# Kernel tuning notes

Hardware: AMD Instinct MI355X
Metric: run time of the kernel (lower is better)

Reference implementation:

```python
import jax, jax.numpy as jnp
import numpy as np

DOWNSAMPLE = 1  # downsample_factor


def _grid(out_h, out_w):
    # rows: x in [-1,1] along width, y in [-1,1] along height, ones
    x_t = jnp.linspace(-1.0, 1.0, out_w, dtype=jnp.float32)
    y_t = jnp.linspace(-1.0, 1.0, out_h, dtype=jnp.float32)
    xg = jnp.tile(x_t[None, :], (out_h, 1)).reshape(-1)
    yg = jnp.tile(y_t[:, None], (1, out_w)).reshape(-1)
    return jnp.stack([xg, yg, jnp.ones_like(xg)], axis=0)  # [3, P]


def spatial_transform(X, theta):
    B, C, H, W = X.shape
    out_h, out_w = H // DOWNSAMPLE, W // DOWNSAMPLE
    grid = _grid(out_h, out_w)                               # [3, P]
    Tg = jnp.einsum('bij,jp->bip', theta.reshape(B, 2, 3), grid)  # [B,2,P]
    x_s, y_s = Tg[:, 0], Tg[:, 1]                            # [B, P]

    # map from [-1,1] to pixel coords (same convention as original)
    x = (x_s + 1.0) * (W / 2.0)
    y = (y_s + 1.0) * (H / 2.0)
    x0 = jnp.floor(x).astype(jnp.int32)
    x1 = x0 + 1
    y0 = jnp.floor(y).astype(jnp.int32)
    y1 = y0 + 1
    x0c = jnp.clip(x0, 0, W - 1)
    x1c = jnp.clip(x1, 0, W - 1)
    y0c = jnp.clip(y0, 0, H - 1)
    y1c = jnp.clip(y1, 0, H - 1)

    im = jnp.transpose(X, (0, 2, 3, 1)).reshape(B, H * W, C)  # [B, HW, C]

    def gather(yi, xi):
        idx = yi * W + xi                                      # [B, P]
        return jnp.take_along_axis(im, idx[:, :, None], axis=1)  # [B, P, C]

    Ia = gather(y0c, x0c)
    Ib = gather(y1c, x0c)
    Ic = gather(y0c, x1c)
    Id = gather(y1c, x1c)

    x0f = x0c.astype(jnp.float32)
    x1f = x1c.astype(jnp.float32)
    y0f = y0c.astype(jnp.float32)
    y1f = y1c.astype(jnp.float32)
    wa = ((x1f - x) * (y1f - y))[:, :, None]
    wb = ((x1f - x) * (y - y0f))[:, :, None]
    wc = ((x - x0f) * (y1f - y))[:, :, None]
    wd = ((x - x0f) * (y - y0f))[:, :, None]

    out = wa * Ia + wb * Ib + wc * Ic + wd * Id               # [B, P, C]
    out = out.reshape(B, out_h, out_w, C)
    return jnp.transpose(out, (0, 3, 1, 2))                   # NCHW


def setup_inputs() -> dict:
    key = jax.random.key(0)
    kx, kt = jax.random.split(key)
    X = jax.random.normal(kx, (32, 3, 512, 512), dtype=jnp.float32)
    # theta near identity + noise for sensible transforms
    ident = jnp.array([1.0, 0.0, 0.0, 0.0, 1.0, 0.0], dtype=jnp.float32)
    theta = ident[None, :] + 0.1 * jax.random.normal(kt, (32, 6), dtype=jnp.float32)
    return {"X": X, "theta": theta}


def reference(X, theta):
    return spatial_transform(X, theta)
```

## Files before the change

### kernel.cpp

```cpp
#include <hip/hip_runtime.h>


#define ST_H 512
#define ST_W 512
#define ST_C 3
#define ST_HW (ST_H * ST_W)

typedef float f2 __attribute__((ext_vector_type(2)));
struct __attribute__((packed, aligned(4))) f2_a4 { f2 v; };

__global__ __launch_bounds__(256) void st_bilinear_kernel(
    const float* __restrict__ X,
    const float* __restrict__ theta,
    float* __restrict__ out,
    int chunk)
{
    int bid = blockIdx.x;
    bid = (bid & 7) * chunk + (bid >> 3);

    const int b   = bid >> 9;
    const int idx = bid & 511;
    const int tx  = idx & 7;
    const int ty  = idx >> 3;

    const int tid = (int)threadIdx.x;
    const int w  = (tx << 6) + (tid & 63);
    const int r  = tid >> 6;
    const int h1 = (ty << 3) + r;
    const int h2 = h1 + 4;

    const float* t = theta + b * 6;
    const float t00 = t[0], t01 = t[1], t02 = t[2];
    const float t10 = t[3], t11 = t[4], t12 = t[5];

    const float STEP = (float)(2.0 / 511.0);
    const float xg  = fmaf((float)w, STEP, -1.0f);
    const float xb0 = fmaf(t00, xg, t02);
    const float yb0 = fmaf(t10, xg, t12);

    const float* __restrict__ Xb = X + (size_t)b * (ST_C * ST_HW);
    float* __restrict__ ob = out + (size_t)b * (ST_C * ST_HW) + w;

#pragma unroll
    for (int k = 0; k < 2; ++k) {
        const int h = k ? h2 : h1;
        const float yg = fmaf((float)h, STEP, -1.0f);
        const float x = (fmaf(t01, yg, xb0) + 1.0f) * 256.0f;
        const float y = (fmaf(t11, yg, yb0) + 1.0f) * 256.0f;

        const int x0 = (int)floorf(x);
        const int y0 = (int)floorf(y);

        const int x0c = min(max(x0, 0), ST_W - 1);
        const int x1c = min(max(x0 + 1, 0), ST_W - 1);
        const int y0c = min(max(y0, 0), ST_H - 1);
        const int y1c = min(max(y0 + 1, 0), ST_H - 1);

        const float x0f = (float)x0c, x1f = (float)x1c;
        const float y0f = (float)y0c, y1f = (float)y1c;
        const float wa = (x1f - x) * (y1f - y);
        const float wb = (x1f - x) * (y - y0f);
        const float wc = (x - x0f) * (y1f - y);
        const float wd = (x - x0f) * (y - y0f);

        const int xa = min(max(x0, 0), ST_W - 2);
        const bool hi = (x0 >= ST_W - 1);
        const bool lo = (x0 < 0);

        const int ia = y0c * ST_W + xa;
        const int ib = y1c * ST_W + xa;

        float* __restrict__ o = ob + h * ST_W;
#pragma unroll
        for (int c = 0; c < ST_C; ++c) {
            const float* __restrict__ Xc = Xb + c * ST_HW;
            const f2 p = ((const f2_a4*)(Xc + ia))->v;
            const f2 q = ((const f2_a4*)(Xc + ib))->v;
            const float Ia = hi ? p.y : p.x;
            const float Ic = lo ? p.x : p.y;
            const float Ib = hi ? q.y : q.x;
            const float Id = lo ? q.x : q.y;
            const float v = wa * Ia + wb * Ib + wc * Ic + wd * Id;
            __builtin_nontemporal_store(v, o + c * ST_HW);
        }
    }
}

extern "C" void kernel_launch(void* const* d_in, const int* in_sizes, int n_in,
                              void* d_out, int out_size, void* d_ws, size_t ws_size,
                              hipStream_t stream) {
    const float* X     = (const float*)d_in[0];
    const float* theta = (const float*)d_in[1];
    float* out         = (float*)d_out;

    const int B = in_sizes[1] / 6;
    const int block = 256;
    const int grid = B * 512;
    const int chunk = grid / 8;

    st_bilinear_kernel<<<grid, block, 0, stream>>>(X, theta, out, chunk);
}
```

Before: 39.40 us.

## Stage output tile in LDS and write with 128-bit nontemporal stores

Each block now covers a 64x16 output tile instead of 64x8, with four rows per thread, and halves the grid. Results are written into shared memory first and then stored to global memory as float4 nontemporal stores, replacing the scalar per-channel stores. The goal is fewer, wider store transactions and fewer blocks, at the cost of 12 KB of LDS per block, a __syncthreads barrier, and less store overlap with the gather loads.

After: 40.97 us. 4.0% more time.

```diff
diff --git a/kernel.cpp b/kernel.cpp
--- a/kernel.cpp
+++ b/kernel.cpp
@@ -7,6 +7,7 @@
 #define ST_HW (ST_H * ST_W)
 
 typedef float f2 __attribute__((ext_vector_type(2)));
+typedef float f4 __attribute__((ext_vector_type(4)));
 struct __attribute__((packed, aligned(4))) f2_a4 { f2 v; };
 
 __global__ __launch_bounds__(256) void st_bilinear_kernel(
@@ -15,19 +16,21 @@
     float* __restrict__ out,
     int chunk)
 {
+    __shared__ float sb[ST_C * 16 * 64];
+
     int bid = blockIdx.x;
     bid = (bid & 7) * chunk + (bid >> 3);
 
-    const int b   = bid >> 9;
-    const int idx = bid & 511;
+    const int b   = bid >> 8;
+    const int idx = bid & 255;
     const int tx  = idx & 7;
     const int ty  = idx >> 3;
+    const int hb  = ty << 4;
 
-    const int tid = (int)threadIdx.x;
-    const int w  = (tx << 6) + (tid & 63);
-    const int r  = tid >> 6;
-    const int h1 = (ty << 3) + r;
-    const int h2 = h1 + 4;
+    const int tid  = (int)threadIdx.x;
+    const int lane = tid & 63;
+    const int r    = tid >> 6;
+    const int w    = (tx << 6) + lane;
 
     const float* t = theta + b * 6;
     const float t00 = t[0], t01 = t[1], t02 = t[2];
@@ -39,11 +42,11 @@
     const float yb0 = fmaf(t10, xg, t12);
 
     const float* __restrict__ Xb = X + (size_t)b * (ST_C * ST_HW);
-    float* __restrict__ ob = out + (size_t)b * (ST_C * ST_HW) + w;
 
 #pragma unroll
-    for (int k = 0; k < 2; ++k) {
-        const int h = k ? h2 : h1;
+    for (int k = 0; k < 4; ++k) {
+        const int row = r + (k << 2);
+        const int h = hb + row;
         const float yg = fmaf((float)h, STEP, -1.0f);
         const float x = (fmaf(t01, yg, xb0) + 1.0f) * 256.0f;
         const float y = (fmaf(t11, yg, yb0) + 1.0f) * 256.0f;
@@ -70,7 +73,6 @@
         const int ia = y0c * ST_W + xa;
         const int ib = y1c * ST_W + xa;
 
-        float* __restrict__ o = ob + h * ST_W;
 #pragma unroll
         for (int c = 0; c < ST_C; ++c) {
             const float* __restrict__ Xc = Xb + c * ST_HW;
@@ -80,9 +82,24 @@
             const float Ic = lo ? p.x : p.y;
             const float Ib = hi ? q.y : q.x;
             const float Id = lo ? q.x : q.y;
-            const float v = wa * Ia + wb * Ib + wc * Ic + wd * Id;
-            __builtin_nontemporal_store(v, o + c * ST_HW);
+            sb[(c * 16 + row) * 64 + lane] =
+                wa * Ia + wb * Ib + wc * Ic + wd * Id;
         }
+    }
+
+    __syncthreads();
+
+    float* __restrict__ ob = out + (size_t)b * (ST_C * ST_HW);
+#pragma unroll
+    for (int k = 0; k < 3; ++k) {
+        const int f = (k * 256 + tid) * 4;
+        const int c = f >> 10;
+        const int rem = f & 1023;
+        const int row = rem >> 6;
+        const int col = rem & 63;
+        const f4 v = *(const f4*)&sb[f];
+        __builtin_nontemporal_store(
+            v, (f4*)(ob + c * ST_HW + (hb + row) * ST_W + (tx << 6) + col));
     }
 }
 
@@ -95,7 +112,7 @@
 
     const int B = in_sizes[1] / 6;
     const int block = 256;
-    const int grid = B * 512;
+    const int grid = B * 256;
     const int chunk = grid / 8;
 
     st_bilinear_kernel<<<grid, block, 0, stream>>>(X, theta, out, chunk);
```
